# Kernel optimization log

Hardware: AMD Instinct MI355X
Metric: run time of the kernel (lower is better)

Reference implementation:

```python
import jax, jax.numpy as jnp
import numpy as np
import math

# quantum-number configuration (matches init_kwargs N=4, L=3, M=3)
N_Q, L_Q, M_Q = 4, 3, 3
OUTC, INC = 16, 16
OUTN, CONV_N = 4096, 27  # output grid points, 3x3x3 conv stencil


def _qnums(N, K, M):
    """Enumerate (n, l, m) exactly as DCConv3dKernelUnitPolynomials._Polynomial_initial."""
    lst = []
    for n in range(1, N + 1):
        for l in range(0, min(n, K + 1)):
            for m in range(-l, l + 1):
                if abs(m) <= M:
                    lst.append((n, l, m))
    return lst

QNUMS = _qnums(N_Q, L_Q, M_Q)
NUM_BASIS = len(QNUMS)  # 30


def _laguerre_coeffs(k, alpha):
    # generalized Laguerre L_k^alpha coefficients, ascending powers
    return [((-1.0) ** i) * math.comb(k + alpha, k - i) / math.factorial(i) for i in range(k + 1)]


def _horner(coeffs_ascending, x):
    acc = jnp.zeros_like(x) + coeffs_ascending[-1]
    for c in reversed(coeffs_ascending[:-1]):
        acc = acc * x + c
    return acc


def _plm(l, m, x):
    """Associated Legendre P_l^m(x) with Condon-Shortley phase, static l,m>=0."""
    somx2 = jnp.sqrt(jnp.clip(1.0 - x * x, 0.0))
    pmm = jnp.ones_like(x)
    for i in range(m):
        pmm = pmm * (-(2.0 * i + 1.0)) * somx2
    if l == m:
        return pmm
    pmmp1 = x * (2.0 * m + 1.0) * pmm
    if l == m + 1:
        return pmmp1
    for ll in range(m + 2, l + 1):
        pll = ((2.0 * ll - 1.0) * x * pmmp1 - (ll + m - 1.0) * pmm) / (ll - m)
        pmm, pmmp1 = pmmp1, pll
    return pmmp1


def _hwfr(n, l, m, r, theta, phi):
    """Real hydrogen wavefunction psi_{nlm}(r, theta, phi), Bohr radius = 1."""
    # radial part R_{nl}
    norm_r = math.sqrt((2.0 / n) ** 3 * math.factorial(n - l - 1) / (2.0 * n * math.factorial(n + l)))
    rho = (2.0 / n) * r
    R = norm_r * jnp.exp(-0.5 * rho) * (rho ** l) * _horner(_laguerre_coeffs(n - l - 1, 2 * l + 1), rho)
    # real spherical harmonic Y_{lm}
    am = abs(m)
    k_lm = math.sqrt((2.0 * l + 1.0) / (4.0 * math.pi) * math.factorial(l - am) / math.factorial(l + am))
    P = _plm(l, am, jnp.cos(theta))
    if m > 0:
        Y = math.sqrt(2.0) * k_lm * P * jnp.cos(am * phi)
    elif m < 0:
        Y = math.sqrt(2.0) * k_lm * P * jnp.sin(am * phi)
    else:
        Y = k_lm * P
    return R * Y


def _basis(position):
    # position: (OutN, conv_n, 3) -> (OutN, conv_n, B)
    r, theta, phi = position[..., 0], position[..., 1], position[..., 2]
    return jnp.stack([_hwfr(n, l, m, r, theta, phi) for (n, l, m) in QNUMS], axis=-1)


def setup_inputs() -> dict:
    key = jax.random.key(0)
    k1, k2, k3, k4 = jax.random.split(key, 4)
    r = 5.0 * jax.random.uniform(k1, (OUTN, CONV_N), dtype=jnp.float32)
    theta = jnp.pi * jax.random.uniform(k2, (OUTN, CONV_N), dtype=jnp.float32)
    phi = 2.0 * jnp.pi * jax.random.uniform(k3, (OUTN, CONV_N), dtype=jnp.float32)
    position = jnp.stack([r, theta, phi], axis=-1)  # (OutN, conv_n, 3)
    coeffs = jax.random.normal(k4, (OUTC, INC, NUM_BASIS), dtype=jnp.float32)
    return {"position": position, "coeffs": coeffs}


def reference(position, coeffs):
    # bas: (OutN, conv_n, B); coeffs: (OutC, InC, B) -> (OutC, InC, OutN, conv_n)
    bas = _basis(position)
    return jnp.einsum("xnb,oib->oixn", bas, coeffs)
```

## Files before the change

### kernel.cpp

```cpp
#include <hip/hip_runtime.h>
#include <math.h>

#define OUTN  4096
#define CONVN 27
#define NPTS  (OUTN * CONVN)
#define NPAIR (NPTS / 2)
#define NB    30
#define NOI   256
#define OI_CHUNK 128
#define NCHUNK (NOI / OI_CHUNK)

typedef float floatx2 __attribute__((ext_vector_type(2)));

__device__ __forceinline__ void eval_basis(float r, float theta, float phi,
                                           float* __restrict__ bas)
{
    const float ct = cosf(theta);
    const float st = sqrtf(fmaxf(1.0f - ct * ct, 0.0f));
    float s1, c1;
    sincosf(phi, &s1, &c1);
    const float c2 = c1 * c1 - s1 * s1;
    const float s2 = 2.0f * c1 * s1;
    const float c3 = c2 * c1 - s2 * s1;
    const float s3 = s2 * c1 + c2 * s1;

    const float P11 = -st;
    const float P20 = 0.5f * (3.0f * ct * ct - 1.0f);
    const float P21 = -3.0f * ct * st;
    const float P22 = 3.0f * (1.0f - ct * ct);
    const float P30 = 0.5f * ct * (5.0f * ct * ct - 3.0f);
    const float P31 = -1.5f * (5.0f * ct * ct - 1.0f) * st;
    const float P32 = 15.0f * ct * (1.0f - ct * ct);
    const float P33 = -15.0f * st * st * st;

    const float PI   = 3.14159265358979323846f;
    const float K00  = sqrtf(1.0f / (4.0f * PI));
    const float K10  = sqrtf(3.0f / (4.0f * PI));
    const float SK11 = sqrtf(2.0f) * sqrtf(3.0f / (8.0f * PI));
    const float K20  = sqrtf(5.0f / (4.0f * PI));
    const float SK21 = sqrtf(2.0f) * sqrtf(5.0f / (24.0f * PI));
    const float SK22 = sqrtf(2.0f) * sqrtf(5.0f / (96.0f * PI));
    const float K30  = sqrtf(7.0f / (4.0f * PI));
    const float SK31 = sqrtf(2.0f) * sqrtf(7.0f / (48.0f * PI));
    const float SK32 = sqrtf(2.0f) * sqrtf(7.0f / (480.0f * PI));
    const float SK33 = sqrtf(2.0f) * sqrtf(7.0f / (2880.0f * PI));

    const float Y00  = K00;
    const float Y1m1 = SK11 * P11 * s1;
    const float Y10  = K10 * ct;
    const float Y1p1 = SK11 * P11 * c1;
    const float Y2m2 = SK22 * P22 * s2;
    const float Y2m1 = SK21 * P21 * s1;
    const float Y20  = K20 * P20;
    const float Y2p1 = SK21 * P21 * c1;
    const float Y2p2 = SK22 * P22 * c2;
    const float Y3m3 = SK33 * P33 * s3;
    const float Y3m2 = SK32 * P32 * s2;
    const float Y3m1 = SK31 * P31 * s1;
    const float Y30  = K30 * P30;
    const float Y3p1 = SK31 * P31 * c1;
    const float Y3p2 = SK32 * P32 * c2;
    const float Y3p3 = SK33 * P33 * c3;

    const float e1 = expf(-r);
    const float e2 = expf(-0.5f * r);
    const float e3 = expf(-r * (1.0f / 3.0f));
    const float e4 = expf(-0.25f * r);
    const float q2 = r;
    const float q3 = (2.0f / 3.0f) * r;
    const float q4 = 0.5f * r;

    const float R10 = 2.0f * e1;
    const float R20 = sqrtf(1.0f / 8.0f)       * e2 * (2.0f - q2);
    const float R21 = sqrtf(1.0f / 24.0f)      * e2 * q2;
    const float R30 = sqrtf(8.0f / 486.0f)     * e3 * (3.0f - 3.0f * q3 + 0.5f * q3 * q3);
    const float R31 = sqrtf(8.0f / 3888.0f)    * e3 * q3 * (4.0f - q3);
    const float R32 = sqrtf(8.0f / 19440.0f)   * e3 * q3 * q3;
    const float R40 = 0.0625f                  * e4 * (4.0f - 6.0f * q4 + 2.0f * q4 * q4 - q4 * q4 * q4 * (1.0f / 6.0f));
    const float R41 = sqrtf(0.25f / 960.0f)    * e4 * q4 * (10.0f - 5.0f * q4 + 0.5f * q4 * q4);
    const float R42 = sqrtf(0.125f / 5760.0f)  * e4 * q4 * q4 * (6.0f - q4);
    const float R43 = sqrtf(0.125f / 40320.0f) * e4 * q4 * q4 * q4;

    bas[0]  = R10 * Y00;
    bas[1]  = R20 * Y00;
    bas[2]  = R21 * Y1m1;
    bas[3]  = R21 * Y10;
    bas[4]  = R21 * Y1p1;
    bas[5]  = R30 * Y00;
    bas[6]  = R31 * Y1m1;
    bas[7]  = R31 * Y10;
    bas[8]  = R31 * Y1p1;
    bas[9]  = R32 * Y2m2;
    bas[10] = R32 * Y2m1;
    bas[11] = R32 * Y20;
    bas[12] = R32 * Y2p1;
    bas[13] = R32 * Y2p2;
    bas[14] = R40 * Y00;
    bas[15] = R41 * Y1m1;
    bas[16] = R41 * Y10;
    bas[17] = R41 * Y1p1;
    bas[18] = R42 * Y2m2;
    bas[19] = R42 * Y2m1;
    bas[20] = R42 * Y20;
    bas[21] = R42 * Y2p1;
    bas[22] = R42 * Y2p2;
    bas[23] = R43 * Y3m3;
    bas[24] = R43 * Y3m2;
    bas[25] = R43 * Y3m1;
    bas[26] = R43 * Y30;
    bas[27] = R43 * Y3p1;
    bas[28] = R43 * Y3p2;
    bas[29] = R43 * Y3p3;
}

__global__ __launch_bounds__(256)
void dcconv_fused(const float* __restrict__ pos,
                  const float* __restrict__ coeffs,
                  float* __restrict__ out)
{
    const int pair = blockIdx.x * 256 + threadIdx.x;
    const int oi0  = blockIdx.y * OI_CHUNK;

    const floatx2* pv = reinterpret_cast<const floatx2*>(pos) + pair * 3;
    const floatx2 pv0 = pv[0], pv1 = pv[1], pv2 = pv[2];

    float basA[NB], basB[NB];
    eval_basis(pv0.x, pv0.y, pv1.x, basA);
    eval_basis(pv1.y, pv2.x, pv2.y, basB);

    floatx2 bas2[NB];
    #pragma unroll
    for (int b = 0; b < NB; ++b) { bas2[b].x = basA[b]; bas2[b].y = basB[b]; }

    floatx2* outp = reinterpret_cast<floatx2*>(out) + pair;
    #pragma unroll 4
    for (int k = 0; k < OI_CHUNK; ++k) {
        const float* cf = coeffs + (size_t)(oi0 + k) * NB;
        floatx2 acc = (floatx2)(0.0f);
        #pragma unroll
        for (int b = 0; b < NB; ++b) {
            const float c = cf[b];
            floatx2 cv; cv.x = c; cv.y = c;
            acc = __builtin_elementwise_fma(cv, bas2[b], acc);
        }
        __builtin_nontemporal_store(acc, &outp[(size_t)(oi0 + k) * NPAIR]);
    }
}

extern "C" void kernel_launch(void* const* d_in, const int* in_sizes, int n_in,
                              void* d_out, int out_size, void* d_ws, size_t ws_size,
                              hipStream_t stream) {
    const float* pos    = (const float*)d_in[0];
    const float* coeffs = (const float*)d_in[1];
    float* out = (float*)d_out;

    dim3 grid(NPAIR / 256, NCHUNK);
    dim3 block(256);
    dcconv_fused<<<grid, block, 0, stream>>>(pos, coeffs, out);
}
```

Measured before the change: 33.82 us.

## Shrink output-channel chunk and process two point-pairs per thread sequentially

Cuts the output-channel chunk per block from 128 to 32. Each thread now handles two point-pairs half the grid apart, evaluating the basis and doing the einsum for one pair, then repeating for the second. This reshapes the grid into more, smaller blocks so work spreads more evenly across CUs, and lets the second basis evaluation overlap with the first pair's outstanding stores. In exchange, each point's basis is recomputed more times in total, since there are four times as many channel chunks.

New measurement: 36.96 us (median of 4 runs). 1.09x slower.

```diff
diff --git a/kernel.cpp b/kernel.cpp
--- a/kernel.cpp
+++ b/kernel.cpp
@@ -5,9 +5,10 @@
 #define CONVN 27
 #define NPTS  (OUTN * CONVN)
 #define NPAIR (NPTS / 2)
+#define NHALF (NPAIR / 2)
 #define NB    30
 #define NOI   256
-#define OI_CHUNK 128
+#define OI_CHUNK 32
 #define NCHUNK (NOI / OI_CHUNK)
 
 typedef float floatx2 __attribute__((ext_vector_type(2)));
@@ -113,26 +114,15 @@
     bas[29] = R43 * Y3p3;
 }
 
-__global__ __launch_bounds__(256)
-void dcconv_fused(const float* __restrict__ pos,
-                  const float* __restrict__ coeffs,
-                  float* __restrict__ out)
+__device__ __forceinline__ void einsum_phase(const float* __restrict__ basA,
+                                             const float* __restrict__ basB,
+                                             const float* __restrict__ coeffs,
+                                             int oi0, floatx2* __restrict__ outp)
 {
-    const int pair = blockIdx.x * 256 + threadIdx.x;
-    const int oi0  = blockIdx.y * OI_CHUNK;
-
-    const floatx2* pv = reinterpret_cast<const floatx2*>(pos) + pair * 3;
-    const floatx2 pv0 = pv[0], pv1 = pv[1], pv2 = pv[2];
-
-    float basA[NB], basB[NB];
-    eval_basis(pv0.x, pv0.y, pv1.x, basA);
-    eval_basis(pv1.y, pv2.x, pv2.y, basB);
-
     floatx2 bas2[NB];
     #pragma unroll
     for (int b = 0; b < NB; ++b) { bas2[b].x = basA[b]; bas2[b].y = basB[b]; }
 
-    floatx2* outp = reinterpret_cast<floatx2*>(out) + pair;
     #pragma unroll 4
     for (int k = 0; k < OI_CHUNK; ++k) {
         const float* cf = coeffs + (size_t)(oi0 + k) * NB;
@@ -147,6 +137,38 @@
     }
 }
 
+__global__ __launch_bounds__(256)
+void dcconv_fused2(const float* __restrict__ pos,
+                   const float* __restrict__ coeffs,
+                   float* __restrict__ out)
+{
+    const int q   = blockIdx.x * 256 + threadIdx.x;
+    const int oi0 = blockIdx.y * OI_CHUNK;
+
+    const int pair1 = q;
+    const int pair2 = q + NHALF;
+
+    float basA[NB], basB[NB];
+
+    {
+        const floatx2* pv = reinterpret_cast<const floatx2*>(pos) + pair1 * 3;
+        const floatx2 pv0 = pv[0], pv1 = pv[1], pv2 = pv[2];
+        eval_basis(pv0.x, pv0.y, pv1.x, basA);
+        eval_basis(pv1.y, pv2.x, pv2.y, basB);
+    }
+    einsum_phase(basA, basB, coeffs, oi0,
+                 reinterpret_cast<floatx2*>(out) + pair1);
+
+    {
+        const floatx2* pv = reinterpret_cast<const floatx2*>(pos) + pair2 * 3;
+        const floatx2 pv0 = pv[0], pv1 = pv[1], pv2 = pv[2];
+        eval_basis(pv0.x, pv0.y, pv1.x, basA);
+        eval_basis(pv1.y, pv2.x, pv2.y, basB);
+    }
+    einsum_phase(basA, basB, coeffs, oi0,
+                 reinterpret_cast<floatx2*>(out) + pair2);
+}
+
 extern "C" void kernel_launch(void* const* d_in, const int* in_sizes, int n_in,
                               void* d_out, int out_size, void* d_ws, size_t ws_size,
                               hipStream_t stream) {
@@ -154,7 +176,7 @@
     const float* coeffs = (const float*)d_in[1];
     float* out = (float*)d_out;
 
-    dim3 grid(NPAIR / 256, NCHUNK);
+    dim3 grid(NHALF / 256, NCHUNK);
     dim3 block(256);
-    dcconv_fused<<<grid, block, 0, stream>>>(pos, coeffs, out);
+    dcconv_fused2<<<grid, block, 0, stream>>>(pos, coeffs, out);
 }
```
